# Optimization experiments

Measured on AMD Instinct MI355X. Metric: run time of the kernel, lower is better.

## Reference

```python
import jax, jax.numpy as jnp
import numpy as np

B, T, DK, DV = 64, 2048, 128, 128
INIT_SCALE = 0.01


def setup_inputs() -> dict:
    key = jax.random.key(0)
    ks = jax.random.split(key, 7)
    return {
        "query": jax.random.normal(ks[0], (B, T, DK), dtype=jnp.float32),
        "key": jax.random.normal(ks[1], (B, T, DK), dtype=jnp.float32),
        "value": jax.random.normal(ks[2], (B, T, DV), dtype=jnp.float32),
        "alpha": jax.random.uniform(ks[3], (B, T, 1), dtype=jnp.float32),
        "rho": jax.random.uniform(ks[4], (B, T, 1), dtype=jnp.float32),
        "lam": jax.random.uniform(ks[5], (B, T, 1), dtype=jnp.float32),
        "init_state": jax.random.normal(ks[6], (B, DK, DV), dtype=jnp.float32) * INIT_SCALE,
    }


def reference(query, key, value, alpha, rho, lam, init_state):
    """Decayed outer-product fast-weight memory, scanned over time.

    Per step t:  M_t = lam_t * M_{t-1} + (rho_t * alpha_t) * (k_t outer v_t)
                 r_t = q_t^T M_t                      # [B, D_v]
    Returns readouts [B, T, D_v].
    """
    # time-major inputs for scan: [T, B, ...]
    tm = lambda x: jnp.swapaxes(x, 0, 1)
    xs = (tm(query), tm(key), tm(value), tm(alpha), tm(rho), tm(lam))

    def step(M, inp):
        q, k, v, a, r, l = inp  # q,k: [B,DK]; v: [B,DV]; a,r,l: [B,1]
        write_scale = (r * a)[:, :, None]          # [B,1,1]
        outer = k[:, :, None] * v[:, None, :]      # [B,DK,DV]
        M = l[:, :, None] * M + write_scale * outer
        read = jnp.einsum('bk,bkv->bv', q, M)      # [B,DV]
        return M, read

    _, reads = jax.lax.scan(step, init_state, xs)
    return jnp.swapaxes(reads, 0, 1)  # [B,T,DV]
```

## Files before the change

### kernel.cpp

```cpp
#include <hip/hip_runtime.h>
#include <hip/hip_bf16.h>


typedef float  f32x4  __attribute__((ext_vector_type(4)));
typedef short  bf16x8 __attribute__((ext_vector_type(8)));
typedef short  bf16x4 __attribute__((ext_vector_type(4)));

constexpr int B_ = 64, T_ = 2048;
constexpr int NSPLIT = 4;
constexpr int CT = 64;
constexpr int NCH = T_ / CT;

__device__ __forceinline__ bf16x8 cvt8(float4 a, float4 b) {
  union { __hip_bfloat162 h2[4]; bf16x8 v; } u;
  u.h2[0] = __float22bfloat162_rn(make_float2(a.x, a.y));
  u.h2[1] = __float22bfloat162_rn(make_float2(a.z, a.w));
  u.h2[2] = __float22bfloat162_rn(make_float2(b.x, b.y));
  u.h2[3] = __float22bfloat162_rn(make_float2(b.z, b.w));
  return u.v;
}

__device__ __forceinline__ float fexp2(float x) { return __builtin_exp2f(x); }
__device__ __forceinline__ float flog2(float x) { return __builtin_log2f(x); }

__device__ __forceinline__ int xk_of(int row) {
  return (row & 7) ^ (((row >> 3) & 3) << 3);
}

#define MFMA(a, b, c) __builtin_amdgcn_mfma_f32_16x16x32_bf16((a), (b), (c), 0, 0, 0)

__device__ __forceinline__ void gload16(const float* gsrc, float* ldst) {
  __builtin_amdgcn_global_load_lds(
      (const __attribute__((address_space(1))) void*)gsrc,
      (__attribute__((address_space(3))) void*)ldst, 16, 0, 0);
}

__global__ __launch_bounds__(512, 1) void lmm_w8(
    const float* __restrict__ q_g, const float* __restrict__ k_g,
    const float* __restrict__ v_g, const float* __restrict__ a_g,
    const float* __restrict__ r_g, const float* __restrict__ l_g,
    const float* __restrict__ m0_g, float* __restrict__ out_g)
{
  const int bid   = blockIdx.y * NSPLIT + blockIdx.x;
  const int b     = (bid & 7) * 8 + (bid >> 5);
  const int split = (bid >> 3) & 3;

  const int tid   = threadIdx.x;
  const int w     = tid >> 6;
  const int lane  = tid & 63;
  const int m     = lane & 15;
  const int quad  = lane >> 4;
  const int tw    = w >> 1;
  const int half  = w & 1;
  const int jbase = split * 32;

  __shared__ __align__(16) float klds[2][64][128];
  __shared__ __align__(16) __hip_bfloat16 MhT [32][136];
  __shared__ __align__(16) __hip_bfloat16 VwT [32][72];
  __shared__ __align__(16) __hip_bfloat16 VwTd[32][72];
  __shared__ __align__(16) __hip_bfloat16 Sd[4][16][72];

  const float* qb = q_g + (size_t)b * T_ * 128;
  const float* kb = k_g + (size_t)b * T_ * 128;
  const float* vb = v_g + (size_t)b * T_ * 128;
  const float* ab = a_g + (size_t)b * T_;
  const float* rb = r_g + (size_t)b * T_;
  const float* lb = l_g + (size_t)b * T_;
  float*       ob = out_g + (size_t)b * T_ * 128;

  f32x4 M[2];
  #pragma unroll
  for (int jt = 0; jt < 2; ++jt)
    #pragma unroll
    for (int r = 0; r < 4; ++r)
      M[jt][r] = m0_g[((size_t)b * 128 + w * 16 + quad * 4 + r) * 128 +
                      jbase + jt * 16 + m];

  const int jv   = tid & 31;
  const int s8   = tid >> 5;
  const int prow = lane >> 5;
  const int pblk = lane & 31;

  float4 qpre[4][2];
  float  vpre[4];
  float  lpre, apre, rpre;

  lpre = lb[lane]; apre = ab[lane]; rpre = rb[lane];
  #pragma unroll
  for (int c = 0; c < 4; ++c) {
    const int row = w * 8 + c * 2 + prow;
    gload16(kb + (size_t)row * 128 + ((pblk ^ xk_of(row)) << 2),
            &klds[0][w * 8 + c * 2][0]);
  }
  #pragma unroll
  for (int ks = 0; ks < 4; ++ks) {
    const float* p = qb + (size_t)(tw * 16 + m) * 128 + ks * 32 + quad * 8;
    qpre[ks][0] = *(const float4*)p;
    qpre[ks][1] = *(const float4*)(p + 4);
  }
  #pragma unroll
  for (int rep = 0; rep < 4; ++rep)
    vpre[rep] = vb[(size_t)(s8 * 4 + rep) * 128 + jbase + jv];

  #pragma unroll 2
  for (int ch = 0; ch < NCH; ++ch) {
    const int t0   = ch * CT;
    const int tn   = (ch + 1 < NCH) ? t0 + CT : t0;
    const int buf  = ch & 1;
    const int nbuf = buf ^ 1;

    __syncthreads();

    #pragma unroll
    for (int c = 0; c < 4; ++c) {
      const int row = w * 8 + c * 2 + prow;
      gload16(kb + (size_t)(tn + row) * 128 + ((pblk ^ xk_of(row)) << 2),
              &klds[nbuf][w * 8 + c * 2][0]);
    }

    float x = flog2(fmaxf(lpre, 1e-20f));
    #pragma unroll
    for (int d = 1; d < 64; d <<= 1) {
      const float o = __shfl_up(x, d, 64);
      if (lane >= d) x += o;
    }
    const float L2    = x;
    const float L2end = __shfl(L2, 63, 64);
    const float arp   = apre * rpre;

    bf16x8 qf[4];
    #pragma unroll
    for (int ks = 0; ks < 4; ++ks) qf[ks] = cvt8(qpre[ks][0], qpre[ks][1]);

    const int tl0 = tw * 16 + quad * 4;
    float tl[4];
    #pragma unroll
    for (int r = 0; r < 4; ++r) tl[r] = __shfl(L2, tl0 + r, 64);

    float fw[4], fd[4];
    #pragma unroll
    for (int rep = 0; rep < 4; ++rep) {
      const int   s   = s8 * 4 + rep;
      const float arf = __shfl(arp, s, 64);
      const float dcf = fexp2(L2end - __shfl(L2, s, 64));
      fw[rep] = vpre[rep] * arf;
      fd[rep] = fw[rep] * dcf;
    }

    lpre = lb[tn + lane]; apre = ab[tn + lane]; rpre = rb[tn + lane];
    #pragma unroll
    for (int ks = 0; ks < 4; ++ks) {
      const float* p = qb + (size_t)(tn + tw * 16 + m) * 128 + ks * 32 + quad * 8;
      qpre[ks][0] = *(const float4*)p;
      qpre[ks][1] = *(const float4*)(p + 4);
    }
    #pragma unroll
    for (int rep = 0; rep < 4; ++rep)
      vpre[rep] = vb[(size_t)(tn + s8 * 4 + rep) * 128 + jbase + jv];

    f32x4 S[2] = {{0.f,0.f,0.f,0.f},{0.f,0.f,0.f,0.f}};
    #pragma unroll
    for (int sb = 0; sb < 2; ++sb) {
      const int rowk = half * 32 + sb * 16 + m;
      const int xk   = xk_of(rowk);
      #pragma unroll
      for (int ks = 0; ks < 4; ++ks) {
        const int bk0 = ks * 8 + quad * 2;
        const float4 kA = *(const float4*)&klds[buf][rowk][((bk0      ^ xk) << 2)];
        const float4 kB = *(const float4*)&klds[buf][rowk][(((bk0 + 1) ^ xk) << 2)];
        S[sb] = MFMA(qf[ks], cvt8(kA, kB), S[sb]);
      }
    }

    #pragma unroll
    for (int sb = 0; sb < 2; ++sb) {
      const int   sl_i = half * 32 + sb * 16 + m;
      const float sl   = __shfl(L2, sl_i, 64);
      #pragma unroll
      for (int r = 0; r < 4; ++r) {
        const float dv = (sl_i <= tl0 + r) ? S[sb][r] * fexp2(tl[r] - sl) : 0.f;
        Sd[tw][quad * 4 + r][sl_i] = __float2bfloat16(dv);
      }
    }

    {
      union { __hip_bfloat162 h2[2]; bf16x4 v; } uw, ud;
      uw.h2[0] = __float22bfloat162_rn(make_float2(fw[0], fw[1]));
      uw.h2[1] = __float22bfloat162_rn(make_float2(fw[2], fw[3]));
      ud.h2[0] = __float22bfloat162_rn(make_float2(fd[0], fd[1]));
      ud.h2[1] = __float22bfloat162_rn(make_float2(fd[2], fd[3]));
      *(bf16x4*)&VwT [jv][s8 * 4] = uw.v;
      *(bf16x4*)&VwTd[jv][s8 * 4] = ud.v;
    }

    #pragma unroll
    for (int jt = 0; jt < 2; ++jt) {
      union { __hip_bfloat162 h2[2]; uint2 u; } pk;
      pk.h2[0] = __float22bfloat162_rn(make_float2(M[jt][0], M[jt][1]));
      pk.h2[1] = __float22bfloat162_rn(make_float2(M[jt][2], M[jt][3]));
      *(uint2*)&MhT[jt * 16 + m][w * 16 + quad * 4] = pk.u;
    }

    __syncthreads();

    f32x4 R = {0.f, 0.f, 0.f, 0.f};
    #pragma unroll
    for (int ks = 0; ks < 4; ++ks) {
      const bf16x8 mb = *(const bf16x8*)&MhT[half * 16 + m][ks * 32 + quad * 8];
      R = MFMA(qf[ks], mb, R);
    }
    #pragma unroll
    for (int r = 0; r < 4; ++r) R[r] *= fexp2(tl[r]);

    #pragma unroll
    for (int kk = 0; kk < 2; ++kk) {
      const bf16x8 sa = *(const bf16x8*)&Sd[tw][m][kk * 32 + quad * 8];
      const bf16x8 vw = *(const bf16x8*)&VwT[half * 16 + m][kk * 32 + quad * 8];
      R = MFMA(sa, vw, R);
    }
    #pragma unroll
    for (int r = 0; r < 4; ++r)
      ob[(size_t)(t0 + tw * 16 + quad * 4 + r) * 128 + jbase + half * 16 + m] =
          R[r];

    const float eend = fexp2(L2end);
    #pragma unroll
    for (int jt = 0; jt < 2; ++jt)
      #pragma unroll
      for (int r = 0; r < 4; ++r) M[jt][r] *= eend;
    #pragma unroll
    for (int kk = 0; kk < 2; ++kk) {
      float kv[8];
      #pragma unroll
      for (int u = 0; u < 8; ++u) {
        const int rows = kk * 32 + quad * 8 + u;
        const int col  = w * 16 + m;
        kv[u] = klds[buf][rows][(((col >> 2) ^ xk_of(rows)) << 2) | (col & 3)];
      }
      const bf16x8 af = cvt8(make_float4(kv[0], kv[1], kv[2], kv[3]),
                             make_float4(kv[4], kv[5], kv[6], kv[7]));
      #pragma unroll
      for (int jt = 0; jt < 2; ++jt) {
        const bf16x8 vd = *(const bf16x8*)&VwTd[jt * 16 + m][kk * 32 + quad * 8];
        M[jt] = MFMA(af, vd, M[jt]);
      }
    }
  }
}

extern "C" void kernel_launch(void* const* d_in, const int* in_sizes, int n_in,
                              void* d_out, int out_size, void* d_ws, size_t ws_size,
                              hipStream_t stream) {
  const float* q  = (const float*)d_in[0];
  const float* k  = (const float*)d_in[1];
  const float* v  = (const float*)d_in[2];
  const float* a  = (const float*)d_in[3];
  const float* r  = (const float*)d_in[4];
  const float* l  = (const float*)d_in[5];
  const float* m0 = (const float*)d_in[6];
  float* out = (float*)d_out;

  dim3 grid(NSPLIT, B_);
  lmm_w8<<<grid, 512, 0, stream>>>(q, k, v, a, r, l, m0, out);
}
```

Baseline: 312.8 us.

## Split value dimension eightfold with 256-thread blocks and bf16 key staging in LDS

New measurement: 337.4 us. 7.9% more time.

```diff
diff --git a/kernel.cpp b/kernel.cpp
--- a/kernel.cpp
+++ b/kernel.cpp
@@ -7,7 +7,7 @@
 typedef short  bf16x4 __attribute__((ext_vector_type(4)));
 
 constexpr int B_ = 64, T_ = 2048;
-constexpr int NSPLIT = 4;
+constexpr int NSPLIT = 8;
 constexpr int CT = 64;
 constexpr int NCH = T_ / CT;
 
@@ -23,41 +23,29 @@
 __device__ __forceinline__ float fexp2(float x) { return __builtin_exp2f(x); }
 __device__ __forceinline__ float flog2(float x) { return __builtin_log2f(x); }
 
-__device__ __forceinline__ int xk_of(int row) {
-  return (row & 7) ^ (((row >> 3) & 3) << 3);
-}
-
 #define MFMA(a, b, c) __builtin_amdgcn_mfma_f32_16x16x32_bf16((a), (b), (c), 0, 0, 0)
 
-__device__ __forceinline__ void gload16(const float* gsrc, float* ldst) {
-  __builtin_amdgcn_global_load_lds(
-      (const __attribute__((address_space(1))) void*)gsrc,
-      (__attribute__((address_space(3))) void*)ldst, 16, 0, 0);
-}
-
-__global__ __launch_bounds__(512, 1) void lmm_w8(
+__global__ __launch_bounds__(256, 2) void lmm_2b(
     const float* __restrict__ q_g, const float* __restrict__ k_g,
     const float* __restrict__ v_g, const float* __restrict__ a_g,
     const float* __restrict__ r_g, const float* __restrict__ l_g,
     const float* __restrict__ m0_g, float* __restrict__ out_g)
 {
   const int bid   = blockIdx.y * NSPLIT + blockIdx.x;
-  const int b     = (bid & 7) * 8 + (bid >> 5);
-  const int split = (bid >> 3) & 3;
+  const int b     = (bid & 7) * 8 + (bid >> 6);
+  const int split = (bid >> 3) & 7;
 
   const int tid   = threadIdx.x;
   const int w     = tid >> 6;
   const int lane  = tid & 63;
   const int m     = lane & 15;
   const int quad  = lane >> 4;
-  const int tw    = w >> 1;
-  const int half  = w & 1;
-  const int jbase = split * 32;
-
-  __shared__ __align__(16) float klds[2][64][128];
-  __shared__ __align__(16) __hip_bfloat16 MhT [32][136];
-  __shared__ __align__(16) __hip_bfloat16 VwT [32][72];
-  __shared__ __align__(16) __hip_bfloat16 VwTd[32][72];
+  const int jbase = split * 16;
+
+  __shared__ __align__(16) __hip_bfloat16 klds[2][64][136];
+  __shared__ __align__(16) __hip_bfloat16 MhT [16][136];
+  __shared__ __align__(16) __hip_bfloat16 VwT [16][72];
+  __shared__ __align__(16) __hip_bfloat16 VwTd[16][72];
   __shared__ __align__(16) __hip_bfloat16 Sd[4][16][72];
 
   const float* qb = q_g + (size_t)b * T_ * 128;
@@ -70,37 +58,39 @@
 
   f32x4 M[2];
   #pragma unroll
-  for (int jt = 0; jt < 2; ++jt)
+  for (int it = 0; it < 2; ++it)
     #pragma unroll
     for (int r = 0; r < 4; ++r)
-      M[jt][r] = m0_g[((size_t)b * 128 + w * 16 + quad * 4 + r) * 128 +
-                      jbase + jt * 16 + m];
-
-  const int jv   = tid & 31;
-  const int s8   = tid >> 5;
-  const int prow = lane >> 5;
-  const int pblk = lane & 31;
+      M[it][r] = m0_g[((size_t)b * 128 + w * 32 + it * 16 + quad * 4 + r) * 128 +
+                      jbase + m];
+
+  const int jv   = tid & 15;
+  const int s16  = tid >> 4;
+  const int krow = tid >> 2;
+  const int kc4  = tid & 3;
 
   float4 qpre[4][2];
+  float4 kpre[8];
   float  vpre[4];
   float  lpre, apre, rpre;
 
   lpre = lb[lane]; apre = ab[lane]; rpre = rb[lane];
   #pragma unroll
-  for (int c = 0; c < 4; ++c) {
-    const int row = w * 8 + c * 2 + prow;
-    gload16(kb + (size_t)row * 128 + ((pblk ^ xk_of(row)) << 2),
-            &klds[0][w * 8 + c * 2][0]);
-  }
+  for (int f = 0; f < 8; ++f)
+    kpre[f] = *(const float4*)&kb[(size_t)krow * 128 + kc4 * 32 + f * 4];
   #pragma unroll
   for (int ks = 0; ks < 4; ++ks) {
-    const float* p = qb + (size_t)(tw * 16 + m) * 128 + ks * 32 + quad * 8;
+    const float* p = qb + (size_t)(w * 16 + m) * 128 + ks * 32 + quad * 8;
     qpre[ks][0] = *(const float4*)p;
     qpre[ks][1] = *(const float4*)(p + 4);
   }
   #pragma unroll
   for (int rep = 0; rep < 4; ++rep)
-    vpre[rep] = vb[(size_t)(s8 * 4 + rep) * 128 + jbase + jv];
+    vpre[rep] = vb[(size_t)(s16 * 4 + rep) * 128 + jbase + jv];
+  #pragma unroll
+  for (int g = 0; g < 4; ++g)
+    *(bf16x8*)&klds[0][krow][kc4 * 32 + g * 8] =
+        cvt8(kpre[2 * g], kpre[2 * g + 1]);
 
   #pragma unroll 2
   for (int ch = 0; ch < NCH; ++ch) {
@@ -111,13 +101,6 @@
 
     __syncthreads();
 
-    #pragma unroll
-    for (int c = 0; c < 4; ++c) {
-      const int row = w * 8 + c * 2 + prow;
-      gload16(kb + (size_t)(tn + row) * 128 + ((pblk ^ xk_of(row)) << 2),
-              &klds[nbuf][w * 8 + c * 2][0]);
-    }
-
     float x = flog2(fmaxf(lpre, 1e-20f));
     #pragma unroll
     for (int d = 1; d < 64; d <<= 1) {
@@ -132,81 +115,81 @@
     #pragma unroll
     for (int ks = 0; ks < 4; ++ks) qf[ks] = cvt8(qpre[ks][0], qpre[ks][1]);
 
-    const int tl0 = tw * 16 + quad * 4;
+    const int tl0 = w * 16 + quad * 4;
     float tl[4];
     #pragma unroll
     for (int r = 0; r < 4; ++r) tl[r] = __shfl(L2, tl0 + r, 64);
 
-    float fw[4], fd[4];
-    #pragma unroll
-    for (int rep = 0; rep < 4; ++rep) {
-      const int   s   = s8 * 4 + rep;
-      const float arf = __shfl(arp, s, 64);
-      const float dcf = fexp2(L2end - __shfl(L2, s, 64));
-      fw[rep] = vpre[rep] * arf;
-      fd[rep] = fw[rep] * dcf;
-    }
-
-    lpre = lb[tn + lane]; apre = ab[tn + lane]; rpre = rb[tn + lane];
-    #pragma unroll
-    for (int ks = 0; ks < 4; ++ks) {
-      const float* p = qb + (size_t)(tn + tw * 16 + m) * 128 + ks * 32 + quad * 8;
-      qpre[ks][0] = *(const float4*)p;
-      qpre[ks][1] = *(const float4*)(p + 4);
-    }
-    #pragma unroll
-    for (int rep = 0; rep < 4; ++rep)
-      vpre[rep] = vb[(size_t)(tn + s8 * 4 + rep) * 128 + jbase + jv];
-
-    f32x4 S[2] = {{0.f,0.f,0.f,0.f},{0.f,0.f,0.f,0.f}};
-    #pragma unroll
-    for (int sb = 0; sb < 2; ++sb) {
-      const int rowk = half * 32 + sb * 16 + m;
-      const int xk   = xk_of(rowk);
+    f32x4 S[4] = {{0.f,0.f,0.f,0.f},{0.f,0.f,0.f,0.f},
+                  {0.f,0.f,0.f,0.f},{0.f,0.f,0.f,0.f}};
+    #pragma unroll
+    for (int sb = 0; sb < 4; ++sb) {
+      const int rowk = sb * 16 + m;
       #pragma unroll
       for (int ks = 0; ks < 4; ++ks) {
-        const int bk0 = ks * 8 + quad * 2;
-        const float4 kA = *(const float4*)&klds[buf][rowk][((bk0      ^ xk) << 2)];
-        const float4 kB = *(const float4*)&klds[buf][rowk][(((bk0 + 1) ^ xk) << 2)];
-        S[sb] = MFMA(qf[ks], cvt8(kA, kB), S[sb]);
-      }
-    }
-
-    #pragma unroll
-    for (int sb = 0; sb < 2; ++sb) {
-      const int   sl_i = half * 32 + sb * 16 + m;
+        const bf16x8 kf = *(const bf16x8*)&klds[buf][rowk][ks * 32 + quad * 8];
+        S[sb] = MFMA(qf[ks], kf, S[sb]);
+      }
+    }
+
+    #pragma unroll
+    for (int sb = 0; sb < 4; ++sb) {
+      const int   sl_i = sb * 16 + m;
       const float sl   = __shfl(L2, sl_i, 64);
       #pragma unroll
       for (int r = 0; r < 4; ++r) {
         const float dv = (sl_i <= tl0 + r) ? S[sb][r] * fexp2(tl[r] - sl) : 0.f;
-        Sd[tw][quad * 4 + r][sl_i] = __float2bfloat16(dv);
+        Sd[w][quad * 4 + r][sl_i] = __float2bfloat16(dv);
       }
     }
 
     {
+      float fw[4], fd[4];
+      #pragma unroll
+      for (int rep = 0; rep < 4; ++rep) {
+        const int   s   = s16 * 4 + rep;
+        const float arf = __shfl(arp, s, 64);
+        const float dcf = fexp2(L2end - __shfl(L2, s, 64));
+        fw[rep] = vpre[rep] * arf;
+        fd[rep] = fw[rep] * dcf;
+      }
       union { __hip_bfloat162 h2[2]; bf16x4 v; } uw, ud;
       uw.h2[0] = __float22bfloat162_rn(make_float2(fw[0], fw[1]));
       uw.h2[1] = __float22bfloat162_rn(make_float2(fw[2], fw[3]));
       ud.h2[0] = __float22bfloat162_rn(make_float2(fd[0], fd[1]));
       ud.h2[1] = __float22bfloat162_rn(make_float2(fd[2], fd[3]));
-      *(bf16x4*)&VwT [jv][s8 * 4] = uw.v;
-      *(bf16x4*)&VwTd[jv][s8 * 4] = ud.v;
-    }
-
-    #pragma unroll
-    for (int jt = 0; jt < 2; ++jt) {
+      *(bf16x4*)&VwT [jv][s16 * 4] = uw.v;
+      *(bf16x4*)&VwTd[jv][s16 * 4] = ud.v;
+    }
+
+    #pragma unroll
+    for (int it = 0; it < 2; ++it) {
       union { __hip_bfloat162 h2[2]; uint2 u; } pk;
-      pk.h2[0] = __float22bfloat162_rn(make_float2(M[jt][0], M[jt][1]));
-      pk.h2[1] = __float22bfloat162_rn(make_float2(M[jt][2], M[jt][3]));
-      *(uint2*)&MhT[jt * 16 + m][w * 16 + quad * 4] = pk.u;
+      pk.h2[0] = __float22bfloat162_rn(make_float2(M[it][0], M[it][1]));
+      pk.h2[1] = __float22bfloat162_rn(make_float2(M[it][2], M[it][3]));
+      *(uint2*)&MhT[m][w * 32 + it * 16 + quad * 4] = pk.u;
     }
 
     __syncthreads();
 
+    lpre = lb[tn + lane]; apre = ab[tn + lane]; rpre = rb[tn + lane];
+    #pragma unroll
+    for (int f = 0; f < 8; ++f)
+      kpre[f] = *(const float4*)&kb[(size_t)(tn + krow) * 128 + kc4 * 32 + f * 4];
+    #pragma unroll
+    for (int ks = 0; ks < 4; ++ks) {
+      const float* p = qb + (size_t)(tn + w * 16 + m) * 128 + ks * 32 + quad * 8;
+      qpre[ks][0] = *(const float4*)p;
+      qpre[ks][1] = *(const float4*)(p + 4);
+    }
+    #pragma unroll
+    for (int rep = 0; rep < 4; ++rep)
+      vpre[rep] = vb[(size_t)(tn + s16 * 4 + rep) * 128 + jbase + jv];
+
     f32x4 R = {0.f, 0.f, 0.f, 0.f};
     #pragma unroll
     for (int ks = 0; ks < 4; ++ks) {
-      const bf16x8 mb = *(const bf16x8*)&MhT[half * 16 + m][ks * 32 + quad * 8];
+      const bf16x8 mb = *(const bf16x8*)&MhT[m][ks * 32 + quad * 8];
       R = MFMA(qf[ks], mb, R);
     }
     #pragma unroll
@@ -214,37 +197,36 @@
 
     #pragma unroll
     for (int kk = 0; kk < 2; ++kk) {
-      const bf16x8 sa = *(const bf16x8*)&Sd[tw][m][kk * 32 + quad * 8];
-      const bf16x8 vw = *(const bf16x8*)&VwT[half * 16 + m][kk * 32 + quad * 8];
+      const bf16x8 sa = *(const bf16x8*)&Sd[w][m][kk * 32 + quad * 8];
+      const bf16x8 vw = *(const bf16x8*)&VwT[m][kk * 32 + quad * 8];
       R = MFMA(sa, vw, R);
     }
     #pragma unroll
     for (int r = 0; r < 4; ++r)
-      ob[(size_t)(t0 + tw * 16 + quad * 4 + r) * 128 + jbase + half * 16 + m] =
-          R[r];
+      ob[(size_t)(t0 + w * 16 + quad * 4 + r) * 128 + jbase + m] = R[r];
 
     const float eend = fexp2(L2end);
     #pragma unroll
-    for (int jt = 0; jt < 2; ++jt)
-      #pragma unroll
-      for (int r = 0; r < 4; ++r) M[jt][r] *= eend;
+    for (int it = 0; it < 2; ++it)
+      #pragma unroll
+      for (int r = 0; r < 4; ++r) M[it][r] *= eend;
     #pragma unroll
     for (int kk = 0; kk < 2; ++kk) {
-      float kv[8];
-      #pragma unroll
-      for (int u = 0; u < 8; ++u) {
-        const int rows = kk * 32 + quad * 8 + u;
-        const int col  = w * 16 + m;
-        kv[u] = klds[buf][rows][(((col >> 2) ^ xk_of(rows)) << 2) | (col & 3)];
-      }
-      const bf16x8 af = cvt8(make_float4(kv[0], kv[1], kv[2], kv[3]),
-                             make_float4(kv[4], kv[5], kv[6], kv[7]));
-      #pragma unroll
-      for (int jt = 0; jt < 2; ++jt) {
-        const bf16x8 vd = *(const bf16x8*)&VwTd[jt * 16 + m][kk * 32 + quad * 8];
-        M[jt] = MFMA(af, vd, M[jt]);
-      }
-    }
+      const bf16x8 vd = *(const bf16x8*)&VwTd[m][kk * 32 + quad * 8];
+      #pragma unroll
+      for (int it = 0; it < 2; ++it) {
+        union { __hip_bfloat16 h[8]; bf16x8 v; } ua;
+        #pragma unroll
+        for (int u = 0; u < 8; ++u)
+          ua.h[u] = klds[buf][kk * 32 + quad * 8 + u][w * 32 + it * 16 + m];
+        M[it] = MFMA(ua.v, vd, M[it]);
+      }
+    }
+
+    #pragma unroll
+    for (int g = 0; g < 4; ++g)
+      *(bf16x8*)&klds[nbuf][krow][kc4 * 32 + g * 8] =
+          cvt8(kpre[2 * g], kpre[2 * g + 1]);
   }
 }
 
@@ -261,5 +243,5 @@
   float* out = (float*)d_out;
 
   dim3 grid(NSPLIT, B_);
-  lmm_w8<<<grid, 512, 0, stream>>>(q, k, v, a, r, l, m0, out);
+  lmm_2b<<<grid, 256, 0, stream>>>(q, k, v, a, r, l, m0, out);
 }
```
